# Performance work log

Measured on AMD Instinct MI355X. Metric: run time of the kernel, lower is better.

The kernel has to match this reference:

```python
import jax, jax.numpy as jnp
import numpy as np

B, C, F, D = 128, 16, 128, 512


def setup_inputs() -> dict:
    key = jax.random.key(0)
    k1, k2 = jax.random.split(key)
    return {
        "c_feats": jax.random.normal(k1, (B, C, D), dtype=jnp.float32),
        "f_feats": jax.random.normal(k2, (B, F, D), dtype=jnp.float32),
    }


def _dtw_path_masks(S):
    """S: [P, c, f] per-pair similarity. Returns [P, c, f] 0/1 max-path masks.

    DP: D[i,j] = max(D[i-1,j], D[i,j-1], D[i-1,j-1]) + S[i-1,j-1], D[0,0]=0,
    borders -inf. Tie-break priority (up, left, diag) matches Python max().
    Row recurrence is vectorized: D[i,j] = Csum[j] + cummax_k<=j(A[k]-Csum[k-1])
    where A[k]=max(D[i-1,k], D[i-1,k-1]) (wavefront-free row-parallel form).
    """
    P_, c, f = S.shape
    NEG = -jnp.inf

    init = jnp.concatenate([jnp.zeros((P_, 1), S.dtype),
                            jnp.full((P_, f), NEG, S.dtype)], axis=1)  # D[0, 0..f]

    def row_step(prev, dt_row):
        # prev: [P, f+1] = D[i-1, 0..f]; dt_row: [P, f] = S[i-1, :]
        A = jnp.maximum(prev[:, 1:], prev[:, :-1])                  # max(D[i-1,j], D[i-1,j-1])
        Ccum = jnp.cumsum(dt_row, axis=1)
        Cm1 = jnp.concatenate([jnp.zeros((P_, 1), dt_row.dtype), Ccum[:, :-1]], axis=1)
        row = Ccum + jax.lax.cummax(A - Cm1, axis=1)                # D[i, 1..f]
        new_prev = jnp.concatenate([jnp.full((P_, 1), NEG, dt_row.dtype), row], axis=1)
        return new_prev, new_prev

    _, rows = jax.lax.scan(row_step, init, jnp.moveaxis(S, 1, 0))   # [c, P, f+1]
    Dm = jnp.moveaxis(jnp.concatenate([init[None], rows], axis=0), 1, 0)  # [P, c+1, f+1]

    # Predecessor choice per cell; argmax picks first max -> priority up,left,diag
    up = Dm[:, :-1, 1:]
    left = Dm[:, 1:, :-1]
    diag = Dm[:, :-1, :-1]
    mv = jnp.argmax(jnp.stack([up, left, diag], axis=-1), axis=-1).astype(jnp.int32)
    mv = jnp.pad(mv, ((0, 0), (1, 0), (1, 0)))                      # [P, c+1, f+1]

    pidx = jnp.arange(P_)

    def bt_step(carry, _):
        mask, i, j = carry
        active = (i > 0) | (j > 0)
        mask = mask.at[pidx, i - 1, j - 1].add(jnp.where(active, 1.0, 0.0).astype(mask.dtype))
        m = mv[pidx, i, j]
        di = jnp.where(m == 1, 0, 1)   # left keeps i
        dj = jnp.where(m == 0, 0, 1)   # up keeps j
        i = jnp.where(active, i - di, i)
        j = jnp.where(active, j - dj, j)
        return (mask, i, j), None

    mask0 = jnp.zeros((P_, c, f), jnp.float32)
    i0 = jnp.full((P_,), c, jnp.int32)
    j0 = jnp.full((P_,), f, jnp.int32)
    (mask, _, _), _ = jax.lax.scan(bt_step, (mask0, i0, j0), None, length=c + f)
    return mask


def reference(c_feats, f_feats):
    b, c, d = c_feats.shape
    f = f_feats.shape[1]
    xn = c_feats / jnp.linalg.norm(c_feats, axis=-1, keepdims=True)
    yn = f_feats / jnp.linalg.norm(f_feats, axis=-1, keepdims=True)
    # Source quirk: y row j is normalized only once outer index i reaches it
    # (y[i-1] bug), so S[i,j] uses normalized y[j] iff j <= i, raw y[j] otherwise.
    Sn = jnp.einsum('mcd,nfd->mncf', xn, yn)
    Sr = jnp.einsum('mcd,nfd->mncf', xn, f_feats)
    tri = jnp.arange(f)[None, :] <= jnp.arange(c)[:, None]          # [c, f]: j <= i
    S = jnp.where(tri, Sn, Sr).reshape(b * b, c, f)
    return _dtw_path_masks(S).reshape(b, b, c, f)
```

## Files before the change

### kernel.cpp

```cpp
#include <hip/hip_runtime.h>
#include <stdint.h>

#define M_TOT 2048
#define N_TOT 16384
#define K_TOT 512

typedef _Float16 f16x8 __attribute__((ext_vector_type(8)));
typedef float f32x16 __attribute__((ext_vector_type(16)));

#define AS1 __attribute__((address_space(1)))
#define AS3 __attribute__((address_space(3)))

__device__ __forceinline__ void ld_lds16(const void* g, void* l) {
    __builtin_amdgcn_global_load_lds((const AS1 void*)g, (AS3 void*)l, 16, 0, 0);
}

#define BAR() do { asm volatile("" ::: "memory"); __builtin_amdgcn_s_barrier(); asm volatile("" ::: "memory"); } while (0)
#define VMC4() asm volatile("s_waitcnt vmcnt(4)" ::: "memory")
#define VMC0() asm volatile("s_waitcnt vmcnt(0)" ::: "memory")

__device__ __forceinline__ void split4(float x0, float x1, float x2, float x3,
                                       uint2* hs, uint2* ls) {
    union U { _Float16 h[4]; uint2 u; } H, L;
    _Float16 h0 = (_Float16)x0; H.h[0] = h0; L.h[0] = (_Float16)(x0 - (float)h0);
    _Float16 h1 = (_Float16)x1; H.h[1] = h1; L.h[1] = (_Float16)(x1 - (float)h1);
    _Float16 h2 = (_Float16)x2; H.h[2] = h2; L.h[2] = (_Float16)(x2 - (float)h2);
    _Float16 h3 = (_Float16)x3; H.h[3] = h3; L.h[3] = (_Float16)(x3 - (float)h3);
    *hs = H.u; *ls = L.u;
}

__global__ __launch_bounds__(256) void norm_split_kernel(
    const float* __restrict__ c_feats, const float* __restrict__ f_feats,
    _Float16* __restrict__ Ah, _Float16* __restrict__ Al,
    _Float16* __restrict__ Bh, _Float16* __restrict__ Bl,
    float* __restrict__ normf)
{
    int wave = blockIdx.x * 4 + (threadIdx.x >> 6);
    int lane = threadIdx.x & 63;
    if (wave < 2048) {
        const float* row = c_feats + (size_t)wave * K_TOT;
        float4 v0 = ((const float4*)row)[lane];
        float4 v1 = ((const float4*)row)[lane + 64];
        double ss = (double)v0.x * v0.x + (double)v0.y * v0.y +
                    (double)v0.z * v0.z + (double)v0.w * v0.w +
                    (double)v1.x * v1.x + (double)v1.y * v1.y +
                    (double)v1.z * v1.z + (double)v1.w * v1.w;
        #pragma unroll
        for (int off = 32; off; off >>= 1) ss += __shfl_down(ss, off);
        double tot = __shfl(ss, 0);
        float nrm = sqrtf((float)tot);
        float a0 = v0.x / nrm, a1 = v0.y / nrm, a2 = v0.z / nrm, a3 = v0.w / nrm;
        float b0 = v1.x / nrm, b1 = v1.y / nrm, b2 = v1.z / nrm, b3 = v1.w / nrm;
        uint2 h, l;
        split4(a0, a1, a2, a3, &h, &l);
        ((uint2*)(Ah + (size_t)wave * K_TOT))[lane] = h;
        ((uint2*)(Al + (size_t)wave * K_TOT))[lane] = l;
        split4(b0, b1, b2, b3, &h, &l);
        ((uint2*)(Ah + (size_t)wave * K_TOT))[lane + 64] = h;
        ((uint2*)(Al + (size_t)wave * K_TOT))[lane + 64] = l;
    } else if (wave < 18432) {
        int fr = wave - 2048;
        const float* row = f_feats + (size_t)fr * K_TOT;
        float4 v0 = ((const float4*)row)[lane];
        float4 v1 = ((const float4*)row)[lane + 64];
        double ss = (double)v0.x * v0.x + (double)v0.y * v0.y +
                    (double)v0.z * v0.z + (double)v0.w * v0.w +
                    (double)v1.x * v1.x + (double)v1.y * v1.y +
                    (double)v1.z * v1.z + (double)v1.w * v1.w;
        #pragma unroll
        for (int off = 32; off; off >>= 1) ss += __shfl_down(ss, off);
        if (lane == 0) normf[fr] = sqrtf((float)ss);
        uint2 h, l;
        split4(v0.x, v0.y, v0.z, v0.w, &h, &l);
        ((uint2*)(Bh + (size_t)fr * K_TOT))[lane] = h;
        ((uint2*)(Bl + (size_t)fr * K_TOT))[lane] = l;
        split4(v1.x, v1.y, v1.z, v1.w, &h, &l);
        ((uint2*)(Bh + (size_t)fr * K_TOT))[lane + 64] = h;
        ((uint2*)(Bl + (size_t)fr * K_TOT))[lane + 64] = l;
    }
}

__global__ __launch_bounds__(512, 2) void mfma_gemm_kernel(
    const _Float16* __restrict__ Ah, const _Float16* __restrict__ Al,
    const _Float16* __restrict__ Bh, const _Float16* __restrict__ Bl,
    const float* __restrict__ normf,
    float* __restrict__ out)
{
    __shared__ _Float16 lds[2 * 4 * 8192];

    const int t = threadIdx.x;
    const int w = t >> 6, lane = t & 63;
    const int m32 = lane & 31, kql0 = lane >> 5;
    const int wr = w >> 2, wc = w & 3;
    const int wm = wr * 128, wn = wc * 64;

    const int bx = (int)blockIdx.x;
    const int ntile = ((bx & 7) << 3) | (bx >> 3);
    const int gm0 = (int)blockIdx.y * 256, gn0 = ntile * 256;

    const int rowA = t >> 2;
    const int kq8 = ((t & 3) ^ ((rowA >> 1) & 3)) * 8;
    const _Float16* const gA  = Ah + (size_t)(gm0 + rowA) * K_TOT + kq8;
    const _Float16* const gB  = Bh + (size_t)(gn0 + rowA) * K_TOT + kq8;
    const _Float16* const gAl2 = gA + (size_t)M_TOT * K_TOT;
    const _Float16* const gBl2 = gB + (size_t)N_TOT * K_TOT;
    const int t8 = t * 8;

    int aof[4][2], bof[2][2];
    #pragma unroll
    for (int mi = 0; mi < 4; ++mi) {
        int rr = wm + mi * 32 + m32;
        int x = (rr >> 1) & 3;
        #pragma unroll
        for (int kc = 0; kc < 2; ++kc)
            aof[mi][kc] = rr * 32 + (((kc * 2 + kql0) ^ x) * 8);
    }
    #pragma unroll
    for (int ni = 0; ni < 2; ++ni) {
        int rr = wn + ni * 32 + m32;
        int x = (rr >> 1) & 3;
        #pragma unroll
        for (int kc = 0; kc < 2; ++kc)
            bof[ni][kc] = rr * 32 + (((kc * 2 + kql0) ^ x) * 8);
    }

    f32x16 acc[4][2] = {};

    {
        _Float16* L0 = lds + t8;
        ld_lds16(gA,            L0);
        ld_lds16(gA  + 65536,   L0 + 4096);
        ld_lds16(gBl2,          L0 + 3 * 8192);
        ld_lds16(gBl2 + 65536,  L0 + 3 * 8192 + 4096);
        ld_lds16(gAl2,          L0 + 1 * 8192);
        ld_lds16(gAl2 + 65536,  L0 + 1 * 8192 + 4096);
        ld_lds16(gB,            L0 + 2 * 8192);
        ld_lds16(gB  + 65536,   L0 + 2 * 8192 + 4096);
        VMC4();
        BAR();
    }

    #pragma unroll 1
    for (int tt = 0; tt < 16; ++tt) {
        const int cb = (tt & 1) << 15;
        const _Float16* Lc = lds + cb;
        _Float16* Ln = lds + (cb ^ 32768) + t8;
        const int kk = tt * 32 + 32;
        const bool st = (tt < 15);

        f16x8 faH[4][2], fbH[2][2], faL[4][2], fbL[2][2];

        #pragma unroll
        for (int mi = 0; mi < 4; ++mi)
            #pragma unroll
            for (int kc = 0; kc < 2; ++kc)
                faH[mi][kc] = *(const f16x8*)(Lc + aof[mi][kc]);
        #pragma unroll
        for (int ni = 0; ni < 2; ++ni)
            #pragma unroll
            for (int kc = 0; kc < 2; ++kc)
                fbL[ni][kc] = *(const f16x8*)(Lc + 3 * 8192 + bof[ni][kc]);
        if (st) {
            ld_lds16(gA   + kk,         Ln);
            ld_lds16(gA   + kk + 65536, Ln + 4096);
            ld_lds16(gBl2 + kk,         Ln + 3 * 8192);
            ld_lds16(gBl2 + kk + 65536, Ln + 3 * 8192 + 4096);
        }
        BAR();
        __builtin_amdgcn_s_setprio(1);
        #pragma unroll
        for (int mi = 0; mi < 4; ++mi)
            #pragma unroll
            for (int ni = 0; ni < 2; ++ni)
                #pragma unroll
                for (int kc = 0; kc < 2; ++kc)
                    acc[mi][ni] = __builtin_amdgcn_mfma_f32_32x32x16_f16(
                        faH[mi][kc], fbL[ni][kc], acc[mi][ni], 0, 0, 0);
        __builtin_amdgcn_s_setprio(0);
        if (st) VMC4(); else VMC0();
        BAR();

        #pragma unroll
        for (int mi = 0; mi < 4; ++mi)
            #pragma unroll
            for (int kc = 0; kc < 2; ++kc)
                faL[mi][kc] = *(const f16x8*)(Lc + 1 * 8192 + aof[mi][kc]);
        #pragma unroll
        for (int ni = 0; ni < 2; ++ni)
            #pragma unroll
            for (int kc = 0; kc < 2; ++kc)
                fbH[ni][kc] = *(const f16x8*)(Lc + 2 * 8192 + bof[ni][kc]);
        if (st) {
            ld_lds16(gAl2 + kk,         Ln + 1 * 8192);
            ld_lds16(gAl2 + kk + 65536, Ln + 1 * 8192 + 4096);
            ld_lds16(gB   + kk,         Ln + 2 * 8192);
            ld_lds16(gB   + kk + 65536, Ln + 2 * 8192 + 4096);
        }
        BAR();
        __builtin_amdgcn_s_setprio(1);
        #pragma unroll
        for (int mi = 0; mi < 4; ++mi)
            #pragma unroll
            for (int ni = 0; ni < 2; ++ni)
                #pragma unroll
                for (int kc = 0; kc < 2; ++kc)
                    acc[mi][ni] = __builtin_amdgcn_mfma_f32_32x32x16_f16(
                        faL[mi][kc], fbH[ni][kc], acc[mi][ni], 0, 0, 0);
        __builtin_amdgcn_s_setprio(0);
        BAR();

        __builtin_amdgcn_s_setprio(1);
        #pragma unroll
        for (int mi = 0; mi < 4; ++mi)
            #pragma unroll
            for (int ni = 0; ni < 2; ++ni)
                #pragma unroll
                for (int kc = 0; kc < 2; ++kc)
                    acc[mi][ni] = __builtin_amdgcn_mfma_f32_32x32x16_f16(
                        faH[mi][kc], fbH[ni][kc], acc[mi][ni], 0, 0, 0);
        __builtin_amdgcn_s_setprio(0);
        if (st) VMC4();
        BAR();
    }

    const int rq = 4 * kql0;
    #pragma unroll
    for (int ni = 0; ni < 2; ++ni) {
        const int gc = gn0 + wn + ni * 32 + m32;
        const int nn = gc >> 7;
        const int col = gc & 127;
        const bool cn = (col < 16);
        const float nf = cn ? normf[gc] : 1.f;
        #pragma unroll
        for (int mi = 0; mi < 4; ++mi) {
            #pragma unroll
            for (int reg = 0; reg < 16; ++reg) {
                const int gm = gm0 + wm + mi * 32 + (reg & 3) + 8 * (reg >> 2) + rq;
                const int mm = gm >> 4, ii = gm & 15;
                float v = acc[mi][ni][reg];
                if (cn && col <= ii) v /= nf;
                out[(((size_t)mm * 128 + nn) * 16 + ii) * 128 + col] = v;
            }
        }
    }
}

#define WQS 304
#define WBUF 1216

__device__ __forceinline__ float dpp_shr1_f32(float x) {
    union { float f; int i; } u, v;
    u.f = x;
    v.i = __builtin_amdgcn_update_dpp(u.i, u.i, 0x111, 0xF, 0xF, false);
    return v.f;
}

__global__ __launch_bounds__(64) void dtw_kernel(float* __restrict__ buf)
{
    __shared__ float swin[2 * WBUF];
    __shared__ uint32_t mvw[4][132];
    __shared__ int bounds[4][16];

    const int lane = threadIdx.x & 63;
    const int q = lane >> 4, r = lane & 15;
    const int pbase = (4095 - (int)blockIdx.x) * 4;
    const float4* gbase = (const float4*)(buf + (size_t)pbase * 2048);
    float* sw = swin;
    uint32_t* mvq = &mvw[q][0];

    int gidx[4], lidx[4];
    #pragma unroll
    for (int i = 0; i < 4; ++i) {
        gidx[i] = i * 512 + ((lane >> 2) & 15) * 32 + (lane & 3);
        lidx[i] = i * WQS + ((lane >> 2) & 15) * 18 + (lane & 3) * 4;
    }

#define WSTORE(regs, boff)                                                      \
    {                                                                           \
        _Pragma("unroll")                                                       \
        for (int i = 0; i < 4; ++i) {                                           \
            *(float2*)(sw + (boff) + lidx[i])     = make_float2(regs[i].x, regs[i].y); \
            *(float2*)(sw + (boff) + lidx[i] + 2) = make_float2(regs[i].z, regs[i].w); \
        }                                                                       \
    }
#define WLOAD(regs, win)                                                        \
    {                                                                           \
        _Pragma("unroll")                                                       \
        for (int i = 0; i < 4; ++i) regs[i] = gbase[gidx[i] + (win) * 4];       \
    }

    float4 ga[4], gb[4];
    WLOAD(ga, 0)
    WLOAD(gb, 1)
    WSTORE(ga, 0)
    WSTORE(gb, WBUF)
    WLOAD(ga, 2)
    WLOAD(gb, 3)

    const float NEG = -1e30f;
    float Dp = NEG, rawprev = NEG;
    uint32_t mvbuf = 0;
    int j = -r;
    const int sb = q * WQS + r * 18;

#define DTW_STEP(BOUNDARY)                                                      \
    {                                                                           \
        float upr = dpp_shr1_f32(Dp);                                           \
        float dg = rawprev;                                                     \
        rawprev = upr;                                                          \
        float up = (r == 0) ? NEG : upr;                                        \
        float lf = Dp;                                                          \
        if (BOUNDARY) {                                                         \
            if (j == 0) { lf = NEG; dg = (r == 0) ? 0.0f : NEG; }               \
            else if (r == 0) dg = NEG;                                          \
        } else {                                                                \
            if (r == 0) dg = NEG;                                               \
        }                                                                       \
        float sv = sw[(((j >> 4) & 1) ? WBUF : 0) + sb + (j & 15)];             \
        int m = (up >= lf && up >= dg) ? 0 : ((lf >= dg) ? 1 : 2);              \
        float Dc = fmaxf(up, fmaxf(lf, dg)) + sv;                               \
        if ((unsigned)j < 128u) {                                               \
            mvbuf |= (uint32_t)m << (2 * (j & 15));                             \
            if ((j & 15) == 15) { mvq[r * 8 + (j >> 4)] = mvbuf; mvbuf = 0; }   \
        }                                                                       \
        Dp = Dc;                                                                \
        ++j;                                                                    \
    }

    for (int tt = 0; tt < 16; ++tt) DTW_STEP(true)
    for (int tt = 16; tt < 32; ++tt) DTW_STEP(false)
    WSTORE(ga, 0)      WLOAD(ga, 4)
    for (int tt = 32; tt < 48; ++tt) DTW_STEP(false)
    WSTORE(gb, WBUF)   WLOAD(gb, 5)
    for (int tt = 48; tt < 64; ++tt) DTW_STEP(false)
    WSTORE(ga, 0)      WLOAD(ga, 6)
    for (int tt = 64; tt < 80; ++tt) DTW_STEP(false)
    WSTORE(gb, WBUF)   WLOAD(gb, 7)
    for (int tt = 80; tt < 96; ++tt) DTW_STEP(false)
    WSTORE(ga, 0)
    for (int tt = 96; tt < 112; ++tt) DTW_STEP(false)
    WSTORE(gb, WBUF)
    for (int tt = 112; tt < 143; ++tt) DTW_STEP(false)
#undef DTW_STEP
#undef WSTORE
#undef WLOAD

    __syncthreads();

    if (r == 0) {
        int i = 16, jj = 128, hic = 127;
        int cidx = -1;
        uint32_t word = 0;
        for (int it = 0; it < 160; ++it) {
            if (i <= 0) break;
            int idx = (i - 1) * 8 + ((jj - 1) >> 4);
            if (idx != cidx) { word = mvq[idx]; cidx = idx; }
            int m = (int)((word >> (2 * ((jj - 1) & 15))) & 3u);
            if (m == 1) { --jj; continue; }
            bounds[q][i - 1] = (jj - 1) | (hic << 8);
            if (m == 2) --jj;
            --i;
            hic = jj - 1;
        }
    }
    __syncthreads();

    #pragma unroll 4
    for (int it = 0; it < 32; ++it) {
        int flat = it * 64 + lane;
        int q2 = flat >> 9;
        int rem = flat & 511;
        int ii = rem >> 5;
        int c4 = rem & 31;
        int b = bounds[q2][ii];
        int lo = b & 0xff, hi = (b >> 8) & 0xff;
        int j0 = c4 * 4;
        float4 v;
        v.x = (j0 + 0 >= lo && j0 + 0 <= hi) ? 1.f : 0.f;
        v.y = (j0 + 1 >= lo && j0 + 1 <= hi) ? 1.f : 0.f;
        v.z = (j0 + 2 >= lo && j0 + 2 <= hi) ? 1.f : 0.f;
        v.w = (j0 + 3 >= lo && j0 + 3 <= hi) ? 1.f : 0.f;
        float* tb = buf + (size_t)(pbase + q2) * 2048;
        *(float4*)(tb + ii * 128 + j0) = v;
    }
}

extern "C" void kernel_launch(void* const* d_in, const int* in_sizes, int n_in,
                              void* d_out, int out_size, void* d_ws, size_t ws_size,
                              hipStream_t stream)
{
    const float* c_feats = (const float*)d_in[0];
    const float* f_feats = (const float*)d_in[1];
    float* out = (float*)d_out;

    _Float16* Ah = (_Float16*)d_ws;
    _Float16* Al = Ah + (size_t)M_TOT * K_TOT;
    _Float16* Bh = Al + (size_t)M_TOT * K_TOT;
    _Float16* Bl = Bh + (size_t)N_TOT * K_TOT;
    float* normf = (float*)(Bl + (size_t)N_TOT * K_TOT);

    norm_split_kernel<<<4608, 256, 0, stream>>>(c_feats, f_feats, Ah, Al, Bh, Bl, normf);
    dim3 g(N_TOT / 256, M_TOT / 256);
    mfma_gemm_kernel<<<g, 512, 0, stream>>>(Ah, Al, Bh, Bl, normf, out);
    dtw_kernel<<<4096, 64, 0, stream>>>(out);
}
```

Baseline: 333.4 us.

## Rebalance GEMM stage pipeline into three phases and deepen DTW window prefetch

The split-fp16 GEMM main loop is restructured so the hi/lo A and B tiles are loaded and consumed across three barrier phases with interleaved MFMA groups. Each load is issued earlier relative to its use, and the waitcnt values are adjusted to match, so global-to-LDS traffic overlaps more compute and less time is spent stalled at barriers. In the DTW kernel, four window register buffers replace two, so global loads are issued further ahead of their LDS stores. This costs more registers, and the reordered waitcnt/barrier logic carries a risk of LDS hazards.

```diff
diff --git a/kernel.cpp b/kernel.cpp
--- a/kernel.cpp
+++ b/kernel.cpp
@@ -16,8 +16,7 @@
 }
 
 #define BAR() do { asm volatile("" ::: "memory"); __builtin_amdgcn_s_barrier(); asm volatile("" ::: "memory"); } while (0)
-#define VMC4() asm volatile("s_waitcnt vmcnt(4)" ::: "memory")
-#define VMC0() asm volatile("s_waitcnt vmcnt(0)" ::: "memory")
+#define VMC(N) asm volatile("s_waitcnt vmcnt(" #N ")" ::: "memory")
 
 __device__ __forceinline__ void split4(float x0, float x1, float x2, float x3,
                                        uint2* hs, uint2* ls) {
@@ -100,8 +99,8 @@
 
     const int rowA = t >> 2;
     const int kq8 = ((t & 3) ^ ((rowA >> 1) & 3)) * 8;
-    const _Float16* const gA  = Ah + (size_t)(gm0 + rowA) * K_TOT + kq8;
-    const _Float16* const gB  = Bh + (size_t)(gn0 + rowA) * K_TOT + kq8;
+    const _Float16* const gA   = Ah + (size_t)(gm0 + rowA) * K_TOT + kq8;
+    const _Float16* const gB   = Bh + (size_t)(gn0 + rowA) * K_TOT + kq8;
     const _Float16* const gAl2 = gA + (size_t)M_TOT * K_TOT;
     const _Float16* const gBl2 = gB + (size_t)N_TOT * K_TOT;
     const int t8 = t * 8;
@@ -132,11 +131,11 @@
         ld_lds16(gA  + 65536,   L0 + 4096);
         ld_lds16(gBl2,          L0 + 3 * 8192);
         ld_lds16(gBl2 + 65536,  L0 + 3 * 8192 + 4096);
+        ld_lds16(gB,            L0 + 2 * 8192);
+        ld_lds16(gB  + 65536,   L0 + 2 * 8192 + 4096);
         ld_lds16(gAl2,          L0 + 1 * 8192);
         ld_lds16(gAl2 + 65536,  L0 + 1 * 8192 + 4096);
-        ld_lds16(gB,            L0 + 2 * 8192);
-        ld_lds16(gB  + 65536,   L0 + 2 * 8192 + 4096);
-        VMC4();
+        VMC(4);
         BAR();
     }
 
@@ -148,10 +147,10 @@
         const int kk = tt * 32 + 32;
         const bool st = (tt < 15);
 
-        f16x8 faH[4][2], fbH[2][2], faL[4][2], fbL[2][2];
-
-        #pragma unroll
-        for (int mi = 0; mi < 4; ++mi)
+        f16x8 faH[4][2], faL[4][2], fbH[2][2], fbL[2][2];
+
+        #pragma unroll
+        for (int mi = 0; mi < 2; ++mi)
             #pragma unroll
             for (int kc = 0; kc < 2; ++kc)
                 faH[mi][kc] = *(const f16x8*)(Lc + aof[mi][kc]);
@@ -161,15 +160,13 @@
             for (int kc = 0; kc < 2; ++kc)
                 fbL[ni][kc] = *(const f16x8*)(Lc + 3 * 8192 + bof[ni][kc]);
         if (st) {
-            ld_lds16(gA   + kk,         Ln);
-            ld_lds16(gA   + kk + 65536, Ln + 4096);
-            ld_lds16(gBl2 + kk,         Ln + 3 * 8192);
-            ld_lds16(gBl2 + kk + 65536, Ln + 3 * 8192 + 4096);
+            ld_lds16(gA + kk,         Ln);
+            ld_lds16(gA + kk + 65536, Ln + 4096);
         }
         BAR();
         __builtin_amdgcn_s_setprio(1);
         #pragma unroll
-        for (int mi = 0; mi < 4; ++mi)
+        for (int mi = 0; mi < 2; ++mi)
             #pragma unroll
             for (int ni = 0; ni < 2; ++ni)
                 #pragma unroll
@@ -177,27 +174,66 @@
                     acc[mi][ni] = __builtin_amdgcn_mfma_f32_32x32x16_f16(
                         faH[mi][kc], fbL[ni][kc], acc[mi][ni], 0, 0, 0);
         __builtin_amdgcn_s_setprio(0);
-        if (st) VMC4(); else VMC0();
-        BAR();
-
-        #pragma unroll
-        for (int mi = 0; mi < 4; ++mi)
+        if (st) VMC(4); else VMC(2);
+        BAR();
+
+        #pragma unroll
+        for (int mi = 2; mi < 4; ++mi)
             #pragma unroll
             for (int kc = 0; kc < 2; ++kc)
-                faL[mi][kc] = *(const f16x8*)(Lc + 1 * 8192 + aof[mi][kc]);
+                faH[mi][kc] = *(const f16x8*)(Lc + aof[mi][kc]);
         #pragma unroll
         for (int ni = 0; ni < 2; ++ni)
             #pragma unroll
             for (int kc = 0; kc < 2; ++kc)
                 fbH[ni][kc] = *(const f16x8*)(Lc + 2 * 8192 + bof[ni][kc]);
         if (st) {
+            ld_lds16(gBl2 + kk,         Ln + 3 * 8192);
+            ld_lds16(gBl2 + kk + 65536, Ln + 3 * 8192 + 4096);
+        }
+        BAR();
+        __builtin_amdgcn_s_setprio(1);
+        #pragma unroll
+        for (int mi = 2; mi < 4; ++mi)
+            #pragma unroll
+            for (int ni = 0; ni < 2; ++ni)
+                #pragma unroll
+                for (int kc = 0; kc < 2; ++kc)
+                    acc[mi][ni] = __builtin_amdgcn_mfma_f32_32x32x16_f16(
+                        faH[mi][kc], fbL[ni][kc], acc[mi][ni], 0, 0, 0);
+        #pragma unroll
+        for (int mi = 0; mi < 2; ++mi)
+            #pragma unroll
+            for (int ni = 0; ni < 2; ++ni)
+                #pragma unroll
+                for (int kc = 0; kc < 2; ++kc)
+                    acc[mi][ni] = __builtin_amdgcn_mfma_f32_32x32x16_f16(
+                        faH[mi][kc], fbH[ni][kc], acc[mi][ni], 0, 0, 0);
+        __builtin_amdgcn_s_setprio(0);
+        if (st) VMC(4); else VMC(0);
+        BAR();
+
+        #pragma unroll
+        for (int mi = 0; mi < 4; ++mi)
+            #pragma unroll
+            for (int kc = 0; kc < 2; ++kc)
+                faL[mi][kc] = *(const f16x8*)(Lc + 1 * 8192 + aof[mi][kc]);
+        if (st) {
+            ld_lds16(gB   + kk,         Ln + 2 * 8192);
+            ld_lds16(gB   + kk + 65536, Ln + 2 * 8192 + 4096);
             ld_lds16(gAl2 + kk,         Ln + 1 * 8192);
             ld_lds16(gAl2 + kk + 65536, Ln + 1 * 8192 + 4096);
-            ld_lds16(gB   + kk,         Ln + 2 * 8192);
-            ld_lds16(gB   + kk + 65536, Ln + 2 * 8192 + 4096);
         }
         BAR();
         __builtin_amdgcn_s_setprio(1);
+        #pragma unroll
+        for (int mi = 2; mi < 4; ++mi)
+            #pragma unroll
+            for (int ni = 0; ni < 2; ++ni)
+                #pragma unroll
+                for (int kc = 0; kc < 2; ++kc)
+                    acc[mi][ni] = __builtin_amdgcn_mfma_f32_32x32x16_f16(
+                        faH[mi][kc], fbH[ni][kc], acc[mi][ni], 0, 0, 0);
         #pragma unroll
         for (int mi = 0; mi < 4; ++mi)
             #pragma unroll
@@ -207,19 +243,7 @@
                     acc[mi][ni] = __builtin_amdgcn_mfma_f32_32x32x16_f16(
                         faL[mi][kc], fbH[ni][kc], acc[mi][ni], 0, 0, 0);
         __builtin_amdgcn_s_setprio(0);
-        BAR();
-
-        __builtin_amdgcn_s_setprio(1);
-        #pragma unroll
-        for (int mi = 0; mi < 4; ++mi)
-            #pragma unroll
-            for (int ni = 0; ni < 2; ++ni)
-                #pragma unroll
-                for (int kc = 0; kc < 2; ++kc)
-                    acc[mi][ni] = __builtin_amdgcn_mfma_f32_32x32x16_f16(
-                        faH[mi][kc], fbH[ni][kc], acc[mi][ni], 0, 0, 0);
-        __builtin_amdgcn_s_setprio(0);
-        if (st) VMC4();
+        if (st) VMC(4);
         BAR();
     }
 
@@ -289,13 +313,11 @@
         for (int i = 0; i < 4; ++i) regs[i] = gbase[gidx[i] + (win) * 4];       \
     }
 
-    float4 ga[4], gb[4];
-    WLOAD(ga, 0)
-    WLOAD(gb, 1)
-    WSTORE(ga, 0)
-    WSTORE(gb, WBUF)
-    WLOAD(ga, 2)
-    WLOAD(gb, 3)
+    float4 W0[4], W1[4], W2[4], W3[4];
+    WLOAD(W0, 0) WLOAD(W1, 1) WLOAD(W2, 2) WLOAD(W3, 3)
+    WSTORE(W0, 0)
+    WSTORE(W1, WBUF)
+    WLOAD(W0, 4) WLOAD(W1, 5)
 
     const float NEG = -1e30f;
     float Dp = NEG, rawprev = NEG;
@@ -329,17 +351,17 @@
 
     for (int tt = 0; tt < 16; ++tt) DTW_STEP(true)
     for (int tt = 16; tt < 32; ++tt) DTW_STEP(false)
-    WSTORE(ga, 0)      WLOAD(ga, 4)
+    WSTORE(W2, 0)        WLOAD(W2, 6)
     for (int tt = 32; tt < 48; ++tt) DTW_STEP(false)
-    WSTORE(gb, WBUF)   WLOAD(gb, 5)
+    WSTORE(W3, WBUF)     WLOAD(W3, 7)
     for (int tt = 48; tt < 64; ++tt) DTW_STEP(false)
-    WSTORE(ga, 0)      WLOAD(ga, 6)
+    WSTORE(W0, 0)
     for (int tt = 64; tt < 80; ++tt) DTW_STEP(false)
-    WSTORE(gb, WBUF)   WLOAD(gb, 7)
+    WSTORE(W1, WBUF)
     for (int tt = 80; tt < 96; ++tt) DTW_STEP(false)
-    WSTORE(ga, 0)
+    WSTORE(W2, 0)
     for (int tt = 96; tt < 112; ++tt) DTW_STEP(false)
-    WSTORE(gb, WBUF)
+    WSTORE(W3, WBUF)
     for (int tt = 112; tt < 143; ++tt) DTW_STEP(false)
 #undef DTW_STEP
 #undef WSTORE
```

After: 338.5 us. No clear change (+1.5%).

## Preload all DTW similarity windows into LDS up front and relax final vmcnt wait

Applied to the files above, without the earlier changes.

The DTW kernel now loads all eight 16-column windows of similarity values into an 8x larger LDS buffer before the wavefront recurrence starts. This removes the interleaved double-buffered reload steps from the inner DP loop, which can then run as one straight loop. The cost is more LDS per block, which may lower occupancy, and a longer serial load phase before the DP begins. In the GEMM, the wait at the last K iteration changes from vmcnt(0) to vmcnt(2), which loosens synchronization and could be unsafe if the outstanding-load count is wrong.

```diff
diff --git a/kernel.cpp b/kernel.cpp
--- a/kernel.cpp
+++ b/kernel.cpp
@@ -16,8 +16,7 @@
 }
 
 #define BAR() do { asm volatile("" ::: "memory"); __builtin_amdgcn_s_barrier(); asm volatile("" ::: "memory"); } while (0)
-#define VMC4() asm volatile("s_waitcnt vmcnt(4)" ::: "memory")
-#define VMC0() asm volatile("s_waitcnt vmcnt(0)" ::: "memory")
+#define VMC(N) asm volatile("s_waitcnt vmcnt(" #N ")" ::: "memory")
 
 __device__ __forceinline__ void split4(float x0, float x1, float x2, float x3,
                                        uint2* hs, uint2* ls) {
@@ -100,8 +99,8 @@
 
     const int rowA = t >> 2;
     const int kq8 = ((t & 3) ^ ((rowA >> 1) & 3)) * 8;
-    const _Float16* const gA  = Ah + (size_t)(gm0 + rowA) * K_TOT + kq8;
-    const _Float16* const gB  = Bh + (size_t)(gn0 + rowA) * K_TOT + kq8;
+    const _Float16* const gA   = Ah + (size_t)(gm0 + rowA) * K_TOT + kq8;
+    const _Float16* const gB   = Bh + (size_t)(gn0 + rowA) * K_TOT + kq8;
     const _Float16* const gAl2 = gA + (size_t)M_TOT * K_TOT;
     const _Float16* const gBl2 = gB + (size_t)N_TOT * K_TOT;
     const int t8 = t * 8;
@@ -136,7 +135,7 @@
         ld_lds16(gAl2 + 65536,  L0 + 1 * 8192 + 4096);
         ld_lds16(gB,            L0 + 2 * 8192);
         ld_lds16(gB  + 65536,   L0 + 2 * 8192 + 4096);
-        VMC4();
+        VMC(4);
         BAR();
     }
 
@@ -161,8 +160,8 @@
             for (int kc = 0; kc < 2; ++kc)
                 fbL[ni][kc] = *(const f16x8*)(Lc + 3 * 8192 + bof[ni][kc]);
         if (st) {
-            ld_lds16(gA   + kk,         Ln);
-            ld_lds16(gA   + kk + 65536, Ln + 4096);
+            ld_lds16(gA + kk,         Ln);
+            ld_lds16(gA + kk + 65536, Ln + 4096);
             ld_lds16(gBl2 + kk,         Ln + 3 * 8192);
             ld_lds16(gBl2 + kk + 65536, Ln + 3 * 8192 + 4096);
         }
@@ -177,7 +176,7 @@
                     acc[mi][ni] = __builtin_amdgcn_mfma_f32_32x32x16_f16(
                         faH[mi][kc], fbL[ni][kc], acc[mi][ni], 0, 0, 0);
         __builtin_amdgcn_s_setprio(0);
-        if (st) VMC4(); else VMC0();
+        if (st) VMC(4); else VMC(2);
         BAR();
 
         #pragma unroll
@@ -219,7 +218,7 @@
                     acc[mi][ni] = __builtin_amdgcn_mfma_f32_32x32x16_f16(
                         faH[mi][kc], fbH[ni][kc], acc[mi][ni], 0, 0, 0);
         __builtin_amdgcn_s_setprio(0);
-        if (st) VMC4();
+        if (st) VMC(4);
         BAR();
     }
 
@@ -257,7 +256,7 @@
 
 __global__ __launch_bounds__(64) void dtw_kernel(float* __restrict__ buf)
 {
-    __shared__ float swin[2 * WBUF];
+    __shared__ float swin[8 * WBUF];
     __shared__ uint32_t mvw[4][132];
     __shared__ int bounds[4][16];
 
@@ -289,13 +288,13 @@
         for (int i = 0; i < 4; ++i) regs[i] = gbase[gidx[i] + (win) * 4];       \
     }
 
-    float4 ga[4], gb[4];
-    WLOAD(ga, 0)
-    WLOAD(gb, 1)
-    WSTORE(ga, 0)
-    WSTORE(gb, WBUF)
-    WLOAD(ga, 2)
-    WLOAD(gb, 3)
+    float4 Wa[4], Wb[4], Wc[4], Wd[4];
+    WLOAD(Wa, 0) WLOAD(Wb, 1) WLOAD(Wc, 2) WLOAD(Wd, 3)
+    WSTORE(Wa, 0)         WSTORE(Wb, WBUF)
+    WSTORE(Wc, 2 * WBUF)  WSTORE(Wd, 3 * WBUF)
+    WLOAD(Wa, 4) WLOAD(Wb, 5) WLOAD(Wc, 6) WLOAD(Wd, 7)
+    WSTORE(Wa, 4 * WBUF)  WSTORE(Wb, 5 * WBUF)
+    WSTORE(Wc, 6 * WBUF)  WSTORE(Wd, 7 * WBUF)
 
     const float NEG = -1e30f;
     float Dp = NEG, rawprev = NEG;
@@ -316,7 +315,7 @@
         } else {                                                                \
             if (r == 0) dg = NEG;                                               \
         }                                                                       \
-        float sv = sw[(((j >> 4) & 1) ? WBUF : 0) + sb + (j & 15)];             \
+        float sv = sw[((j >> 4) & 7) * WBUF + sb + (j & 15)];                   \
         int m = (up >= lf && up >= dg) ? 0 : ((lf >= dg) ? 1 : 2);              \
         float Dc = fmaxf(up, fmaxf(lf, dg)) + sv;                               \
         if ((unsigned)j < 128u) {                                               \
@@ -328,19 +327,7 @@
     }
 
     for (int tt = 0; tt < 16; ++tt) DTW_STEP(true)
-    for (int tt = 16; tt < 32; ++tt) DTW_STEP(false)
-    WSTORE(ga, 0)      WLOAD(ga, 4)
-    for (int tt = 32; tt < 48; ++tt) DTW_STEP(false)
-    WSTORE(gb, WBUF)   WLOAD(gb, 5)
-    for (int tt = 48; tt < 64; ++tt) DTW_STEP(false)
-    WSTORE(ga, 0)      WLOAD(ga, 6)
-    for (int tt = 64; tt < 80; ++tt) DTW_STEP(false)
-    WSTORE(gb, WBUF)   WLOAD(gb, 7)
-    for (int tt = 80; tt < 96; ++tt) DTW_STEP(false)
-    WSTORE(ga, 0)
-    for (int tt = 96; tt < 112; ++tt) DTW_STEP(false)
-    WSTORE(gb, WBUF)
-    for (int tt = 112; tt < 143; ++tt) DTW_STEP(false)
+    for (int tt = 16; tt < 143; ++tt) DTW_STEP(false)
 #undef DTW_STEP
 #undef WSTORE
 #undef WLOAD
```

Result: slower. 459.7 us (+37.9%).
